# Kernel tuning notes

Hardware: AMD Instinct MI355X
Metric: run time of the kernel (lower is better)

Reference implementation:

```python
import jax, jax.numpy as jnp
import numpy as np

B, N, C, D = 16, 1024, 768, 384

def setup_inputs() -> dict:
    key = jax.random.key(0)
    ks = jax.random.split(key, 12)
    s_in = 1.0 / np.sqrt(C)
    s_d = 1.0 / np.sqrt(D)
    return {
        "x": jax.random.normal(ks[0], (B, N, C), dtype=jnp.float32),
        "adj": jax.random.uniform(ks[1], (B, N, N), dtype=jnp.float32),
        "W_theta": jax.random.uniform(ks[2], (C, D), minval=-s_in, maxval=s_in),
        "b_theta": jax.random.uniform(ks[3], (D,), minval=-s_in, maxval=s_in),
        "W_phi": jax.random.uniform(ks[4], (C, D), minval=-s_in, maxval=s_in),
        "b_phi": jax.random.uniform(ks[5], (D,), minval=-s_in, maxval=s_in),
        "W_g": jax.random.uniform(ks[6], (C, D), minval=-s_in, maxval=s_in),
        "b_g": jax.random.uniform(ks[7], (D,), minval=-s_in, maxval=s_in),
        "W_out": jax.random.uniform(ks[8], (D, C), minval=-s_d, maxval=s_d),
        "b_out": jax.random.uniform(ks[9], (C,), minval=-s_d, maxval=s_d),
    }

def reference(x, adj, W_theta, b_theta, W_phi, b_phi, W_g, b_g, W_out, b_out):
    # projections: [B,N,C] @ [C,D] -> [B,N,D]
    theta = x @ W_theta + b_theta
    phi = x @ W_phi + b_phi
    g = x @ W_g + b_g
    # unscaled attention scores with multiplicative adjacency mask
    attn = jnp.einsum('bnd,bmd->bnm', theta, phi) * adj  # [B,N,N]
    attn = jax.nn.softmax(attn, axis=-1)  # dropout is identity in eval mode
    out = jnp.einsum('bnm,bmd->bnd', attn, g)  # [B,N,D]
    out = out @ W_out + b_out  # [B,N,C]
    return out + x
```

## Files before the change

### kernel.cpp

```cpp
#include <hip/hip_runtime.h>
#include <hip/hip_bf16.h>

typedef __hip_bfloat16 bf16;
typedef short bf16x8 __attribute__((ext_vector_type(8)));
typedef float f32x4 __attribute__((ext_vector_type(4)));

constexpr int Bb = 16, Nn = 1024, Cc = 768, Dd = 384;

static __device__ __forceinline__ f32x4 mfma16(bf16x8 a, bf16x8 b, f32x4 c) {
    return __builtin_amdgcn_mfma_f32_16x16x32_bf16(a, b, c, 0, 0, 0);
}
static __device__ __forceinline__ short f2b(float v) {
    __hip_bfloat16 h = __float2bfloat16(v);
    return *reinterpret_cast<short*>(&h);
}
static __device__ __forceinline__ unsigned pack2(float lo, float hi) {
    return ((unsigned)(unsigned short)f2b(hi) << 16) | (unsigned short)(unsigned)f2b(lo);
}
static __device__ __forceinline__ float b2f(bf16 x) { return __bfloat162float(x); }

__global__ __launch_bounds__(256) void cast_bias(
    const float* __restrict__ in, uint4* __restrict__ out,
    const float* __restrict__ bt, const float* __restrict__ bp,
    const float* __restrict__ bg, float* __restrict__ biasP)
{
    const size_t i = (size_t)blockIdx.x * 256 + threadIdx.x;
    const float4 a = reinterpret_cast<const float4*>(in)[i * 2];
    const float4 b = reinterpret_cast<const float4*>(in)[i * 2 + 1];
    uint4 v;
    v.x = pack2(a.x, a.y);
    v.y = pack2(a.z, a.w);
    v.z = pack2(b.x, b.y);
    v.w = pack2(b.z, b.w);
    out[i] = v;
    if (blockIdx.x == 0) {
        for (int k = threadIdx.x; k < 1152; k += 256)
            biasP[k] = k < 384 ? bt[k] : (k < 768 ? bp[k - 384] : bg[k - 768]);
    }
}

__global__ __launch_bounds__(256) void transpose_cast(
    const float* __restrict__ in, bf16* __restrict__ out, int K, int N)
{
    __shared__ float t[32][33];
    const int n0 = blockIdx.x * 32, k0 = blockIdx.y * 32;
    const int tx = threadIdx.x & 31, ty = threadIdx.x >> 5;
#pragma unroll
    for (int i = 0; i < 4; i++)
        t[ty + i * 8][tx] = in[(size_t)(k0 + ty + i * 8) * N + n0 + tx];
    __syncthreads();
#pragma unroll
    for (int i = 0; i < 4; i++)
        out[(size_t)(n0 + ty + i * 8) * K + k0 + tx] = __float2bfloat16(t[tx][ty + i * 8]);
}

__global__ __launch_bounds__(256) void transpose_cast3(
    const float* __restrict__ w0, const float* __restrict__ w1,
    const float* __restrict__ w2, bf16* __restrict__ outbase)
{
    __shared__ float t[32][33];
    const float* in = blockIdx.z == 0 ? w0 : (blockIdx.z == 1 ? w1 : w2);
    bf16* out = outbase + (size_t)blockIdx.z * Cc * Dd;
    const int n0 = blockIdx.x * 32, k0 = blockIdx.y * 32;
    const int tx = threadIdx.x & 31, ty = threadIdx.x >> 5;
#pragma unroll
    for (int i = 0; i < 4; i++)
        t[ty + i * 8][tx] = in[(size_t)(k0 + ty + i * 8) * Dd + n0 + tx];
    __syncthreads();
#pragma unroll
    for (int i = 0; i < 4; i++)
        out[(size_t)(n0 + ty + i * 8) * Cc + k0 + tx] = __float2bfloat16(t[tx][ty + i * 8]);
}

template <typename TA, int EPI>
__global__ __launch_bounds__(256) void gemm_mfma(
    const TA* __restrict__ A, const bf16* __restrict__ BT,
    const float* __restrict__ bias, const float* __restrict__ resid,
    void* __restrict__ outp, int K, int Nout)
{
    __shared__ short As[128 * 40];
    __shared__ short Bs[128 * 40];
    const int tid = threadIdx.x;
    const int lane = tid & 63, w = tid >> 6;
    const int quad = lane >> 4, c = lane & 15;
    const int row0 = blockIdx.x * 128, col0 = blockIdx.y * 128;
    const int wm = (w & 1) * 64, wn = (w >> 1) * 64;

    const f32x4 fz = {0.f, 0.f, 0.f, 0.f};
    f32x4 acc[4][4];
#pragma unroll
    for (int i = 0; i < 4; i++)
#pragma unroll
        for (int j = 0; j < 4; j++) acc[i][j] = fz;

    for (int k0 = 0; k0 < K; k0 += 32) {
        __syncthreads();
        if (sizeof(TA) == 4) {
            const float* Af = (const float*)A;
#pragma unroll
            for (int u = 0; u < 4; u++) {
                const int id = u * 256 + tid;
                const int r = id >> 3, c4 = (id & 7) * 4;
                const float4 v = *reinterpret_cast<const float4*>(Af + (size_t)(row0 + r) * K + k0 + c4);
                uint2 p;
                p.x = pack2(v.x, v.y);
                p.y = pack2(v.z, v.w);
                *reinterpret_cast<uint2*>(&As[r * 40 + c4]) = p;
            }
        } else {
            const bf16* Ab = (const bf16*)A;
#pragma unroll
            for (int u = 0; u < 2; u++) {
                const int id = u * 256 + tid;
                const int r = id >> 2, c8 = (id & 3) * 8;
                const uint4 v = *reinterpret_cast<const uint4*>(Ab + (size_t)(row0 + r) * K + k0 + c8);
                *reinterpret_cast<uint4*>(&As[r * 40 + c8]) = v;
            }
        }
#pragma unroll
        for (int u = 0; u < 2; u++) {
            const int id = u * 256 + tid;
            const int r = id >> 2, c8 = (id & 3) * 8;
            const uint4 v = *reinterpret_cast<const uint4*>(BT + (size_t)(col0 + r) * K + k0 + c8);
            *reinterpret_cast<uint4*>(&Bs[r * 40 + c8]) = v;
        }
        __syncthreads();

        bf16x8 af[4], bfr[4];
#pragma unroll
        for (int i = 0; i < 4; i++)
            af[i] = *reinterpret_cast<const bf16x8*>(&As[(wm + i * 16 + c) * 40 + quad * 8]);
#pragma unroll
        for (int j = 0; j < 4; j++)
            bfr[j] = *reinterpret_cast<const bf16x8*>(&Bs[(wn + j * 16 + c) * 40 + quad * 8]);
#pragma unroll
        for (int i = 0; i < 4; i++)
#pragma unroll
            for (int j = 0; j < 4; j++)
                acc[i][j] = mfma16(af[i], bfr[j], acc[i][j]);
    }

    const size_t SZc = (size_t)Bb * Nn * Dd;
#pragma unroll
    for (int i = 0; i < 4; i++) {
        const int rowb = row0 + wm + i * 16 + quad * 4;
#pragma unroll
        for (int j = 0; j < 4; j++) {
            const int col = col0 + wn + j * 16 + c;
            const float bcol = bias[col];
#pragma unroll
            for (int r = 0; r < 4; r++) {
                float v = acc[i][j][r] + bcol;
                const int rr = rowb + r;
                if (EPI == 0) {
                    ((bf16*)outp)[(size_t)rr * Nout + col] = __float2bfloat16(v);
                } else if (EPI == 1) {
                    const int bb = rr >> 10, m = rr & 1023;
                    ((bf16*)outp)[((size_t)(bb * Nout + col)) * 1024 + m] = __float2bfloat16(v);
                } else if (EPI == 2) {
                    v += resid[(size_t)rr * Nout + col];
                    ((float*)outp)[(size_t)rr * Nout + col] = v;
                } else {
                    const int seg = col / 384;
                    const int cl = col - seg * 384;
                    bf16* base = (bf16*)outp;
                    if (seg < 2) {
                        base[(size_t)seg * SZc + (size_t)rr * Dd + cl] = __float2bfloat16(v);
                    } else {
                        const int bb = rr >> 10, m = rr & 1023;
                        base[2 * SZc + ((size_t)(bb * Dd + cl)) * 1024 + m] = __float2bfloat16(v);
                    }
                }
            }
        }
    }
}

template <int SPLIT>
__global__ __launch_bounds__(256, 2) void flash_attn(
    const bf16* __restrict__ theta, const bf16* __restrict__ phi,
    const bf16* __restrict__ gT, const float* __restrict__ adj,
    bf16* __restrict__ O, float* __restrict__ Sp, float* __restrict__ ml)
{
    __shared__ short phs[32 * 392];
    __shared__ short gts[192 * 64];

    const int tid = threadIdx.x;
    const int lane = tid & 63, w = tid >> 6;
    const int quad = lane >> 4, c = lane & 15;
    const int qb = blockIdx.x, b = blockIdx.y;
    const int sp = (SPLIT > 1) ? blockIdx.z : 0;
    constexpr int CH = Nn / SPLIT;
    const int n_lo = sp * CH;

    const size_t thbase = ((size_t)b * Nn + qb * 64 + w * 16 + c) * Dd;
    bf16x8 ath[12];
#pragma unroll
    for (int dq = 0; dq < 12; dq++)
        ath[dq] = *reinterpret_cast<const bf16x8*>(theta + thbase + dq * 32 + quad * 8);

    const int goff = (c >> 1) * 64 + (((4 * (c & 1) + quad) ^ ((c >> 1) & 7)) * 8);

    const f32x4 fz = {0.f, 0.f, 0.f, 0.f};
    f32x4 o[24];
#pragma unroll
    for (int t = 0; t < 24; t++) o[t] = fz;
    float mrow[4], lrow[4];
#pragma unroll
    for (int r = 0; r < 4; r++) { mrow[r] = -INFINITY; lrow[r] = 0.f; }

    for (int it = 0; it < CH / 32; ++it) {
        const int n0 = n_lo + it * 32;
        __syncthreads();
        {
            const bf16* src = phi + ((size_t)b * Nn + n0) * Dd;
#pragma unroll
            for (int u = 0; u < 6; u++) {
                const int id = u * 256 + tid;
                const int r = id / 48, cc = (id % 48) * 8;
                const uint4 v = *reinterpret_cast<const uint4*>(src + (size_t)r * Dd + cc);
                *reinterpret_cast<uint4*>(&phs[r * 392 + cc]) = v;
            }
        }
        {
            const bf16* src = gT + ((size_t)b * Dd) * Nn + n0;
#pragma unroll
            for (int u = 0; u < 6; u++) {
                const int id = u * 256 + tid;
                const int r = id >> 3, sl = id & 7;
                const int sg = sl ^ (r & 7);
                const int d = 2 * r + (sg >> 2), cc = (sg & 3) * 8;
                const uint4 v = *reinterpret_cast<const uint4*>(src + (size_t)d * Nn + cc);
                *reinterpret_cast<uint4*>(&gts[id * 8]) = v;
            }
        }
        __syncthreads();

        f32x4 s0 = fz, s1 = fz;
#pragma unroll
        for (int dq = 0; dq < 12; dq++) {
            const bf16x8 b0 = *reinterpret_cast<const bf16x8*>(&phs[c * 392 + dq * 32 + quad * 8]);
            const bf16x8 b1 = *reinterpret_cast<const bf16x8*>(&phs[(16 + c) * 392 + dq * 32 + quad * 8]);
            s0 = mfma16(ath[dq], b0, s0);
            s1 = mfma16(ath[dq], b1, s1);
        }

        const float* arow = adj + ((size_t)b * Nn + qb * 64 + w * 16 + quad * 4) * Nn + n0;
        float p0[4], p1[4], alpha[4];
#pragma unroll
        for (int r = 0; r < 4; r++) {
            const float v0 = s0[r] * arow[(size_t)r * Nn + c];
            const float v1 = s1[r] * arow[(size_t)r * Nn + 16 + c];
            float t = fmaxf(v0, v1);
#pragma unroll
            for (int msk = 1; msk < 16; msk <<= 1) t = fmaxf(t, __shfl_xor(t, msk));
            const float mn = fmaxf(mrow[r], t);
            alpha[r] = __expf(mrow[r] - mn);
            mrow[r] = mn;
            p0[r] = __expf(v0 - mn);
            p1[r] = __expf(v1 - mn);
            float u = p0[r] + p1[r];
#pragma unroll
            for (int msk = 1; msk < 16; msk <<= 1) u += __shfl_xor(u, msk);
            lrow[r] = lrow[r] * alpha[r] + u;
        }
#pragma unroll
        for (int t = 0; t < 24; t++)
#pragma unroll
            for (int r = 0; r < 4; r++) o[t][r] *= alpha[r];

        __syncthreads();
        short* pl = phs + w * 640;
#pragma unroll
        for (int r = 0; r < 4; r++) {
            pl[(quad * 4 + r) * 40 + c] = f2b(p0[r]);
            pl[(quad * 4 + r) * 40 + 16 + c] = f2b(p1[r]);
        }
        const bf16x8 ap = *reinterpret_cast<const bf16x8*>(&pl[c * 40 + quad * 8]);
#pragma unroll
        for (int dn = 0; dn < 24; dn++) {
            const bf16x8 bg = *reinterpret_cast<const bf16x8*>(&gts[dn * 512 + goff]);
            o[dn] = mfma16(ap, bg, o[dn]);
        }
    }

    const int rowb = qb * 64 + w * 16 + quad * 4;
    if (SPLIT > 1) {
        float* srow = Sp + ((size_t)sp * Bb * Nn + (size_t)b * Nn + rowb) * Dd;
#pragma unroll
        for (int dn = 0; dn < 24; dn++)
#pragma unroll
            for (int r = 0; r < 4; r++)
                srow[(size_t)r * Dd + dn * 16 + c] = o[dn][r];
        if (c == 0) {
#pragma unroll
            for (int r = 0; r < 4; r++) {
                const size_t rid = (size_t)sp * Bb * Nn + (size_t)b * Nn + rowb + r;
                ml[rid * 2]     = mrow[r];
                ml[rid * 2 + 1] = lrow[r];
            }
        }
    } else {
        float inv[4];
#pragma unroll
        for (int r = 0; r < 4; r++) inv[r] = 1.0f / lrow[r];
        bf16* orow = O + ((size_t)b * Nn + rowb) * Dd;
#pragma unroll
        for (int dn = 0; dn < 24; dn++)
#pragma unroll
            for (int r = 0; r < 4; r++)
                orow[(size_t)r * Dd + dn * 16 + c] = __float2bfloat16(o[dn][r] * inv[r]);
    }
}

template <int NS>
__global__ __launch_bounds__(256) void attn_combine(
    const float* __restrict__ Sp, const float* __restrict__ ml,
    bf16* __restrict__ O)
{
    constexpr size_t M = (size_t)Bb * Nn;
    const size_t idx = (size_t)blockIdx.x * 256 + threadIdx.x;
    const size_t e0 = idx * 4;
    const size_t row = e0 / Dd;
    float mv[NS], lv[NS];
    float mx = -INFINITY;
#pragma unroll
    for (int i = 0; i < NS; i++) {
        mv[i] = ml[((size_t)i * M + row) * 2];
        lv[i] = ml[((size_t)i * M + row) * 2 + 1];
        mx = fmaxf(mx, mv[i]);
    }
    float wsum = 0.f, wv[NS];
#pragma unroll
    for (int i = 0; i < NS; i++) { wv[i] = __expf(mv[i] - mx); wsum += wv[i] * lv[i]; }
    const float inv = 1.0f / wsum;
    float ax = 0.f, ay = 0.f, az = 0.f, aw = 0.f;
#pragma unroll
    for (int i = 0; i < NS; i++) {
        const float4 a = *reinterpret_cast<const float4*>(Sp + (size_t)i * M * Dd + e0);
        ax += wv[i] * a.x; ay += wv[i] * a.y; az += wv[i] * a.z; aw += wv[i] * a.w;
    }
    uint2 p;
    p.x = pack2(ax * inv, ay * inv);
    p.y = pack2(az * inv, aw * inv);
    *reinterpret_cast<uint2*>(O + e0) = p;
}

__global__ __launch_bounds__(256) void proj_gemm(
    const float* __restrict__ A, const float* __restrict__ W,
    const float* __restrict__ bias, bf16* __restrict__ out,
    int M, int K, int Nd)
{
    __shared__ float Asm[16][65];
    __shared__ float Bsm[16][65];
    const int tid = threadIdx.x;
    const int tx = tid & 15, ty = tid >> 4;
    const int row0 = blockIdx.x * 64, col0 = blockIdx.y * 64;
    float acc[4][4] = {};
    for (int k0 = 0; k0 < K; k0 += 16) {
        {
            const int m = tid >> 2, kq = (tid & 3) * 4;
            const float* p = A + (size_t)(row0 + m) * K + k0 + kq;
#pragma unroll
            for (int j = 0; j < 4; j++) Asm[kq + j][m] = p[j];
        }
        {
            const int k = tid >> 4, n4 = (tid & 15) * 4;
            const float* p = W + (size_t)(k0 + k) * Nd + col0 + n4;
#pragma unroll
            for (int j = 0; j < 4; j++) Bsm[k][n4 + j] = p[j];
        }
        __syncthreads();
#pragma unroll
        for (int k = 0; k < 16; k++) {
            float a[4], bv[4];
#pragma unroll
            for (int j = 0; j < 4; j++) a[j] = Asm[k][ty * 4 + j];
#pragma unroll
            for (int j = 0; j < 4; j++) bv[j] = Bsm[k][tx * 4 + j];
#pragma unroll
            for (int i = 0; i < 4; i++)
#pragma unroll
                for (int j = 0; j < 4; j++) acc[i][j] += a[i] * bv[j];
        }
        __syncthreads();
    }
#pragma unroll
    for (int i = 0; i < 4; i++) {
        const int row = row0 + ty * 4 + i;
#pragma unroll
        for (int j = 0; j < 4; j++) {
            const int col = col0 + tx * 4 + j;
            out[(size_t)row * Nd + col] = __float2bfloat16(acc[i][j] + bias[col]);
        }
    }
}

__global__ __launch_bounds__(256) void fused_attn(
    const float* __restrict__ x, const float* __restrict__ adj,
    const float* __restrict__ W_theta, const float* __restrict__ b_theta,
    const bf16* __restrict__ phi, const bf16* __restrict__ g,
    const float* __restrict__ W_out, const float* __restrict__ b_out,
    float* __restrict__ out)
{
    __shared__ float xs[Cc];
    __shared__ float th[Dd];
    __shared__ float s[Nn];
    __shared__ float Os[Dd];
    __shared__ float red[256];
    const int tid = threadIdx.x;
    const int n = blockIdx.x, b = blockIdx.y;
    const int lane = tid & 63, wave = tid >> 6;
    const size_t row = (size_t)b * Nn + n;
    const size_t baseD = (size_t)b * Nn * Dd;
    for (int c = tid; c < Cc; c += 256) xs[c] = x[row * Cc + c];
    __syncthreads();
    for (int d = tid; d < Dd; d += 256) {
        float acc = b_theta[d];
#pragma unroll 8
        for (int c = 0; c < Cc; c++) acc += xs[c] * W_theta[(size_t)c * Dd + d];
        th[d] = acc;
    }
    __syncthreads();
    for (int m = wave; m < Nn; m += 4) {
        const bf16* prow = phi + baseD + (size_t)m * Dd;
        float partial = 0.f;
#pragma unroll
        for (int j = 0; j < 6; j++) {
            const int d = lane + 64 * j;
            partial += th[d] * b2f(prow[d]);
        }
#pragma unroll
        for (int off = 32; off > 0; off >>= 1) partial += __shfl_down(partial, off);
        if (lane == 0)
            s[m] = partial * adj[(size_t)b * Nn * Nn + (size_t)n * Nn + m];
    }
    __syncthreads();
    float mx = -1e30f;
    for (int i = tid; i < Nn; i += 256) mx = fmaxf(mx, s[i]);
    red[tid] = mx; __syncthreads();
    for (int st = 128; st > 0; st >>= 1) {
        if (tid < st) red[tid] = fmaxf(red[tid], red[tid + st]);
        __syncthreads();
    }
    mx = red[0]; __syncthreads();
    float lsum = 0.f;
    for (int i = tid; i < Nn; i += 256) {
        const float e = __expf(s[i] - mx);
        s[i] = e;
        lsum += e;
    }
    red[tid] = lsum; __syncthreads();
    for (int st = 128; st > 0; st >>= 1) {
        if (tid < st) red[tid] += red[tid + st];
        __syncthreads();
    }
    const float inv = 1.0f / red[0];
    __syncthreads();
    for (int d = tid; d < Dd; d += 256) {
        float acc = 0.f;
#pragma unroll 8
        for (int m = 0; m < Nn; m++) acc += s[m] * b2f(g[baseD + (size_t)m * Dd + d]);
        Os[d] = acc * inv;
    }
    __syncthreads();
    for (int c = tid; c < Cc; c += 256) {
        float acc = b_out[c] + xs[c];
#pragma unroll 8
        for (int d = 0; d < Dd; d++) acc += Os[d] * W_out[(size_t)d * Cc + c];
        out[row * Cc + c] = acc;
    }
}

extern "C" void kernel_launch(void* const* d_in, const int* in_sizes, int n_in,
                              void* d_out, int out_size, void* d_ws, size_t ws_size,
                              hipStream_t stream)
{
    const float* x       = (const float*)d_in[0];
    const float* adj     = (const float*)d_in[1];
    const float* W_theta = (const float*)d_in[2];
    const float* b_theta = (const float*)d_in[3];
    const float* W_phi   = (const float*)d_in[4];
    const float* b_phi   = (const float*)d_in[5];
    const float* W_g     = (const float*)d_in[6];
    const float* b_g     = (const float*)d_in[7];
    const float* W_out   = (const float*)d_in[8];
    const float* b_out   = (const float*)d_in[9];
    float* out = (float*)d_out;

    const int M = Bb * Nn;
    const size_t SZ  = (size_t)Bb * Nn * Dd;
    const size_t SZX = (size_t)M * Cc;
    const size_t WSZ = (size_t)Cc * Dd;
    const size_t NEED_OLD = (4 * WSZ + 4 * SZ) * sizeof(bf16);
    const size_t NEED_NEW = (4 * WSZ + 4 * SZ + SZX) * sizeof(bf16)
                          + 1152 * sizeof(float);
    const size_t NEED_S2 = NEED_NEW + (2 * SZ + 4 * (size_t)M) * sizeof(float);
    const size_t NEED_S4 = NEED_NEW + (4 * SZ + 8 * (size_t)M) * sizeof(float);

    dim3 blk(256);

    if (ws_size >= NEED_NEW) {
        bf16* WtT   = (bf16*)d_ws;
        bf16* WoT   = WtT + 3 * WSZ;
        bf16* theta = WoT + WSZ;
        bf16* phi   = theta + SZ;
        bf16* gT    = phi + SZ;
        bf16* O     = gT + SZ;
        bf16* xb    = O + SZ;
        float* biasP = (float*)(xb + SZX);
        float* Sp    = biasP + 1152;
        float* mlp   = Sp + 4 * SZ;

        cast_bias<<<dim3((unsigned)(SZX / 2048)), blk, 0, stream>>>(
            x, (uint4*)xb, b_theta, b_phi, b_g, biasP);
        transpose_cast3<<<dim3(Dd / 32, Cc / 32, 3), blk, 0, stream>>>(
            W_theta, W_phi, W_g, WtT);
        transpose_cast<<<dim3(Cc / 32, Dd / 32), blk, 0, stream>>>(W_out, WoT, Dd, Cc);

        gemm_mfma<bf16, 3><<<dim3(M / 128, 1152 / 128), blk, 0, stream>>>(
            xb, WtT, biasP, nullptr, theta, Cc, 1152);

        if (ws_size >= NEED_S4) {
            flash_attn<4><<<dim3(Nn / 64, Bb, 4), blk, 0, stream>>>(
                theta, phi, gT, adj, nullptr, Sp, mlp);
            attn_combine<4><<<dim3((unsigned)(SZ / 1024)), blk, 0, stream>>>(Sp, mlp, O);
        } else if (ws_size >= NEED_S2) {
            float* mlp2 = Sp + 2 * SZ;
            flash_attn<2><<<dim3(Nn / 64, Bb, 2), blk, 0, stream>>>(
                theta, phi, gT, adj, nullptr, Sp, mlp2);
            attn_combine<2><<<dim3((unsigned)(SZ / 1024)), blk, 0, stream>>>(Sp, mlp2, O);
        } else {
            flash_attn<1><<<dim3(Nn / 64, Bb, 1), blk, 0, stream>>>(
                theta, phi, gT, adj, O, nullptr, nullptr);
        }

        gemm_mfma<bf16, 2><<<dim3(M / 128, Cc / 128), blk, 0, stream>>>(
            O, WoT, b_out, x, out, Dd, Cc);
    } else if (ws_size >= NEED_OLD) {
        bf16* WtT   = (bf16*)d_ws;
        bf16* WpT   = WtT + WSZ;
        bf16* WgT   = WtT + 2 * WSZ;
        bf16* WoT   = WtT + 3 * WSZ;
        bf16* theta = WoT + WSZ;
        bf16* phi   = theta + SZ;
        bf16* gT    = phi + SZ;
        bf16* O     = gT + SZ;

        transpose_cast<<<dim3(Dd / 32, Cc / 32), blk, 0, stream>>>(W_theta, WtT, Cc, Dd);
        transpose_cast<<<dim3(Dd / 32, Cc / 32), blk, 0, stream>>>(W_phi,   WpT, Cc, Dd);
        transpose_cast<<<dim3(Dd / 32, Cc / 32), blk, 0, stream>>>(W_g,     WgT, Cc, Dd);
        transpose_cast<<<dim3(Cc / 32, Dd / 32), blk, 0, stream>>>(W_out,   WoT, Dd, Cc);

        dim3 gp(M / 128, Dd / 128);
        gemm_mfma<float, 0><<<gp, blk, 0, stream>>>(x, WtT, b_theta, nullptr, theta, Cc, Dd);
        gemm_mfma<float, 0><<<gp, blk, 0, stream>>>(x, WpT, b_phi,   nullptr, phi,   Cc, Dd);
        gemm_mfma<float, 1><<<gp, blk, 0, stream>>>(x, WgT, b_g,     nullptr, gT,    Cc, Dd);

        flash_attn<1><<<dim3(Nn / 64, Bb, 1), blk, 0, stream>>>(
            theta, phi, gT, adj, O, nullptr, nullptr);

        dim3 go(M / 128, Cc / 128);
        gemm_mfma<bf16, 2><<<go, blk, 0, stream>>>(O, WoT, b_out, x, out, Dd, Cc);
    } else {
        bf16* phi = (bf16*)d_ws;
        bf16* g   = phi + SZ;
        dim3 gproj(M / 64, Dd / 64);
        proj_gemm<<<gproj, blk, 0, stream>>>(x, W_phi, b_phi, phi, M, Cc, Dd);
        proj_gemm<<<gproj, blk, 0, stream>>>(x, W_g, b_g, g, M, Cc, Dd);
        fused_attn<<<dim3(Nn, Bb), blk, 0, stream>>>(
            x, adj, W_theta, b_theta, phi, g, W_out, b_out, out);
    }
}
```

Before: 354.0 us.

## Add direct global-to-LDS bf16 GEMM with XOR swizzle and drop split-4 attention

Adds a new bf16 GEMM kernel that loads A and B tiles straight into LDS with global_load_lds, using a K-step of 64 and an XOR-swizzled layout to avoid bank conflicts. This replaces the register-staged path used for the QKV projection and output GEMMs. It also removes the split-4 attention path, so the default runs split-2 attention with its combine step, which changes how much parallelism the attention stage has. The new GEMM keeps the two-barrier, single-buffer scheme, so loads still do not overlap with compute.

```diff
diff --git a/kernel.cpp b/kernel.cpp
--- a/kernel.cpp
+++ b/kernel.cpp
@@ -18,6 +18,10 @@
     return ((unsigned)(unsigned short)f2b(hi) << 16) | (unsigned short)(unsigned)f2b(lo);
 }
 static __device__ __forceinline__ float b2f(bf16 x) { return __bfloat162float(x); }
+
+#define GLOAD_LDS16(g, l) __builtin_amdgcn_global_load_lds(                    \
+    (const __attribute__((address_space(1))) void*)(g),                        \
+    (__attribute__((address_space(3))) void*)(l), 16, 0, 0)
 
 __global__ __launch_bounds__(256) void cast_bias(
     const float* __restrict__ in, uint4* __restrict__ out,
@@ -72,20 +76,27 @@
         out[(size_t)(n0 + ty + i * 8) * Cc + k0 + tx] = __float2bfloat16(t[tx][ty + i * 8]);
 }
 
-template <typename TA, int EPI>
-__global__ __launch_bounds__(256) void gemm_mfma(
-    const TA* __restrict__ A, const bf16* __restrict__ BT,
+template <int EPI>
+__global__ __launch_bounds__(256) void gemm_bf16(
+    const bf16* __restrict__ A, const bf16* __restrict__ BT,
     const float* __restrict__ bias, const float* __restrict__ resid,
     void* __restrict__ outp, int K, int Nout)
 {
-    __shared__ short As[128 * 40];
-    __shared__ short Bs[128 * 40];
+    __shared__ short As[128 * 64];
+    __shared__ short Bs[128 * 64];
     const int tid = threadIdx.x;
     const int lane = tid & 63, w = tid >> 6;
     const int quad = lane >> 4, c = lane & 15;
     const int row0 = blockIdx.x * 128, col0 = blockIdx.y * 128;
     const int wm = (w & 1) * 64, wn = (w >> 1) * 64;
 
+    const int rA = w * 32 + (lane >> 3);
+    const int cs = (lane & 7) ^ (lane >> 3);
+    const bf16* Ag = A  + (size_t)(row0 + rA) * K + cs * 8;
+    const bf16* Bg = BT + (size_t)(col0 + rA) * K + cs * 8;
+    char* Asb = (char*)As + w * 4096;
+    char* Bsb = (char*)Bs + w * 4096;
+
     const f32x4 fz = {0.f, 0.f, 0.f, 0.f};
     f32x4 acc[4][4];
 #pragma unroll
@@ -93,51 +104,38 @@
 #pragma unroll
         for (int j = 0; j < 4; j++) acc[i][j] = fz;
 
-    for (int k0 = 0; k0 < K; k0 += 32) {
-        __syncthreads();
-        if (sizeof(TA) == 4) {
-            const float* Af = (const float*)A;
-#pragma unroll
-            for (int u = 0; u < 4; u++) {
-                const int id = u * 256 + tid;
-                const int r = id >> 3, c4 = (id & 7) * 4;
-                const float4 v = *reinterpret_cast<const float4*>(Af + (size_t)(row0 + r) * K + k0 + c4);
-                uint2 p;
-                p.x = pack2(v.x, v.y);
-                p.y = pack2(v.z, v.w);
-                *reinterpret_cast<uint2*>(&As[r * 40 + c4]) = p;
-            }
-        } else {
-            const bf16* Ab = (const bf16*)A;
-#pragma unroll
-            for (int u = 0; u < 2; u++) {
-                const int id = u * 256 + tid;
-                const int r = id >> 2, c8 = (id & 3) * 8;
-                const uint4 v = *reinterpret_cast<const uint4*>(Ab + (size_t)(row0 + r) * K + k0 + c8);
-                *reinterpret_cast<uint4*>(&As[r * 40 + c8]) = v;
-            }
-        }
-#pragma unroll
-        for (int u = 0; u < 2; u++) {
-            const int id = u * 256 + tid;
-            const int r = id >> 2, c8 = (id & 3) * 8;
-            const uint4 v = *reinterpret_cast<const uint4*>(BT + (size_t)(col0 + r) * K + k0 + c8);
-            *reinterpret_cast<uint4*>(&Bs[r * 40 + c8]) = v;
-        }
-        __syncthreads();
-
-        bf16x8 af[4], bfr[4];
-#pragma unroll
-        for (int i = 0; i < 4; i++)
-            af[i] = *reinterpret_cast<const bf16x8*>(&As[(wm + i * 16 + c) * 40 + quad * 8]);
-#pragma unroll
-        for (int j = 0; j < 4; j++)
-            bfr[j] = *reinterpret_cast<const bf16x8*>(&Bs[(wn + j * 16 + c) * 40 + quad * 8]);
-#pragma unroll
-        for (int i = 0; i < 4; i++)
-#pragma unroll
-            for (int j = 0; j < 4; j++)
-                acc[i][j] = mfma16(af[i], bfr[j], acc[i][j]);
+    for (int k0 = 0; k0 < K; k0 += 64) {
+        __syncthreads();
+#pragma unroll
+        for (int i = 0; i < 4; i++) {
+            GLOAD_LDS16(Ag + (size_t)i * 8 * K + k0, Asb + i * 1024);
+            GLOAD_LDS16(Bg + (size_t)i * 8 * K + k0, Bsb + i * 1024);
+        }
+        __syncthreads();
+
+        bf16x8 af[2][4], bfr[2][4];
+#pragma unroll
+        for (int kk = 0; kk < 2; kk++) {
+#pragma unroll
+            for (int i = 0; i < 4; i++) {
+                const int r = wm + i * 16 + c;
+                const int ch = (kk * 4 + quad) ^ (r & 7);
+                af[kk][i] = *reinterpret_cast<const bf16x8*>(&As[r * 64 + ch * 8]);
+            }
+#pragma unroll
+            for (int j = 0; j < 4; j++) {
+                const int r = wn + j * 16 + c;
+                const int ch = (kk * 4 + quad) ^ (r & 7);
+                bfr[kk][j] = *reinterpret_cast<const bf16x8*>(&Bs[r * 64 + ch * 8]);
+            }
+        }
+#pragma unroll
+        for (int kk = 0; kk < 2; kk++)
+#pragma unroll
+            for (int i = 0; i < 4; i++)
+#pragma unroll
+                for (int j = 0; j < 4; j++)
+                    acc[i][j] = mfma16(af[kk][i], bfr[kk][j], acc[i][j]);
     }
 
     const size_t SZc = (size_t)Bb * Nn * Dd;
@@ -152,12 +150,7 @@
             for (int r = 0; r < 4; r++) {
                 float v = acc[i][j][r] + bcol;
                 const int rr = rowb + r;
-                if (EPI == 0) {
-                    ((bf16*)outp)[(size_t)rr * Nout + col] = __float2bfloat16(v);
-                } else if (EPI == 1) {
-                    const int bb = rr >> 10, m = rr & 1023;
-                    ((bf16*)outp)[((size_t)(bb * Nout + col)) * 1024 + m] = __float2bfloat16(v);
-                } else if (EPI == 2) {
+                if (EPI == 2) {
                     v += resid[(size_t)rr * Nout + col];
                     ((float*)outp)[(size_t)rr * Nout + col] = v;
                 } else {
@@ -170,6 +163,99 @@
                         const int bb = rr >> 10, m = rr & 1023;
                         base[2 * SZc + ((size_t)(bb * Dd + cl)) * 1024 + m] = __float2bfloat16(v);
                     }
+                }
+            }
+        }
+    }
+}
+
+template <typename TA, int EPI>
+__global__ __launch_bounds__(256) void gemm_mfma(
+    const TA* __restrict__ A, const bf16* __restrict__ BT,
+    const float* __restrict__ bias, const float* __restrict__ resid,
+    void* __restrict__ outp, int K, int Nout)
+{
+    __shared__ short As[128 * 40];
+    __shared__ short Bs[128 * 40];
+    const int tid = threadIdx.x;
+    const int lane = tid & 63, w = tid >> 6;
+    const int quad = lane >> 4, c = lane & 15;
+    const int row0 = blockIdx.x * 128, col0 = blockIdx.y * 128;
+    const int wm = (w & 1) * 64, wn = (w >> 1) * 64;
+
+    const f32x4 fz = {0.f, 0.f, 0.f, 0.f};
+    f32x4 acc[4][4];
+#pragma unroll
+    for (int i = 0; i < 4; i++)
+#pragma unroll
+        for (int j = 0; j < 4; j++) acc[i][j] = fz;
+
+    for (int k0 = 0; k0 < K; k0 += 32) {
+        __syncthreads();
+        if (sizeof(TA) == 4) {
+            const float* Af = (const float*)A;
+#pragma unroll
+            for (int u = 0; u < 4; u++) {
+                const int id = u * 256 + tid;
+                const int r = id >> 3, c4 = (id & 7) * 4;
+                const float4 v = *reinterpret_cast<const float4*>(Af + (size_t)(row0 + r) * K + k0 + c4);
+                uint2 p;
+                p.x = pack2(v.x, v.y);
+                p.y = pack2(v.z, v.w);
+                *reinterpret_cast<uint2*>(&As[r * 40 + c4]) = p;
+            }
+        } else {
+            const bf16* Ab = (const bf16*)A;
+#pragma unroll
+            for (int u = 0; u < 2; u++) {
+                const int id = u * 256 + tid;
+                const int r = id >> 2, c8 = (id & 3) * 8;
+                const uint4 v = *reinterpret_cast<const uint4*>(Ab + (size_t)(row0 + r) * K + k0 + c8);
+                *reinterpret_cast<uint4*>(&As[r * 40 + c8]) = v;
+            }
+        }
+#pragma unroll
+        for (int u = 0; u < 2; u++) {
+            const int id = u * 256 + tid;
+            const int r = id >> 2, c8 = (id & 3) * 8;
+            const uint4 v = *reinterpret_cast<const uint4*>(BT + (size_t)(col0 + r) * K + k0 + c8);
+            *reinterpret_cast<uint4*>(&Bs[r * 40 + c8]) = v;
+        }
+        __syncthreads();
+
+        bf16x8 af[4], bfr[4];
+#pragma unroll
+        for (int i = 0; i < 4; i++)
+            af[i] = *reinterpret_cast<const bf16x8*>(&As[(wm + i * 16 + c) * 40 + quad * 8]);
+#pragma unroll
+        for (int j = 0; j < 4; j++)
+            bfr[j] = *reinterpret_cast<const bf16x8*>(&Bs[(wn + j * 16 + c) * 40 + quad * 8]);
+#pragma unroll
+        for (int i = 0; i < 4; i++)
+#pragma unroll
+            for (int j = 0; j < 4; j++)
+                acc[i][j] = mfma16(af[i], bfr[j], acc[i][j]);
+    }
+
+#pragma unroll
+    for (int i = 0; i < 4; i++) {
+        const int rowb = row0 + wm + i * 16 + quad * 4;
+#pragma unroll
+        for (int j = 0; j < 4; j++) {
+            const int col = col0 + wn + j * 16 + c;
+            const float bcol = bias[col];
+#pragma unroll
+            for (int r = 0; r < 4; r++) {
+                float v = acc[i][j][r] + bcol;
+                const int rr = rowb + r;
+                if (EPI == 0) {
+                    ((bf16*)outp)[(size_t)rr * Nout + col] = __float2bfloat16(v);
+                } else if (EPI == 1) {
+                    const int bb = rr >> 10, m = rr & 1023;
+                    ((bf16*)outp)[((size_t)(bb * Nout + col)) * 1024 + m] = __float2bfloat16(v);
+                } else {
+                    v += resid[(size_t)rr * Nout + col];
+                    ((float*)outp)[(size_t)rr * Nout + col] = v;
                 }
             }
         }
@@ -496,7 +582,6 @@
     const size_t NEED_NEW = (4 * WSZ + 4 * SZ + SZX) * sizeof(bf16)
                           + 1152 * sizeof(float);
     const size_t NEED_S2 = NEED_NEW + (2 * SZ + 4 * (size_t)M) * sizeof(float);
-    const size_t NEED_S4 = NEED_NEW + (4 * SZ + 8 * (size_t)M) * sizeof(float);
 
     dim3 blk(256);
 
@@ -510,7 +595,7 @@
         bf16* xb    = O + SZ;
         float* biasP = (float*)(xb + SZX);
         float* Sp    = biasP + 1152;
-        float* mlp   = Sp + 4 * SZ;
+        float* mlp   = Sp + 2 * SZ;
 
         cast_bias<<<dim3((unsigned)(SZX / 2048)), blk, 0, stream>>>(
             x, (uint4*)xb, b_theta, b_phi, b_g, biasP);
@@ -518,24 +603,19 @@
             W_theta, W_phi, W_g, WtT);
         transpose_cast<<<dim3(Cc / 32, Dd / 32), blk, 0, stream>>>(W_out, WoT, Dd, Cc);
 
-        gemm_mfma<bf16, 3><<<dim3(M / 128, 1152 / 128), blk, 0, stream>>>(
+        gemm_bf16<3><<<dim3(M / 128, 1152 / 128), blk, 0, stream>>>(
             xb, WtT, biasP, nullptr, theta, Cc, 1152);
 
-        if (ws_size >= NEED_S4) {
-            flash_attn<4><<<dim3(Nn / 64, Bb, 4), blk, 0, stream>>>(
+        if (ws_size >= NEED_S2) {
+            flash_attn<2><<<dim3(Nn / 64, Bb, 2), blk, 0, stream>>>(
                 theta, phi, gT, adj, nullptr, Sp, mlp);
-            attn_combine<4><<<dim3((unsigned)(SZ / 1024)), blk, 0, stream>>>(Sp, mlp, O);
-        } else if (ws_size >= NEED_S2) {
-            float* mlp2 = Sp + 2 * SZ;
-            flash_attn<2><<<dim3(Nn / 64, Bb, 2), blk, 0, stream>>>(
-                theta, phi, gT, adj, nullptr, Sp, mlp2);
-            attn_combine<2><<<dim3((unsigned)(SZ / 1024)), blk, 0, stream>>>(Sp, mlp2, O);
+            attn_combine<2><<<dim3((unsigned)(SZ / 1024)), blk, 0, stream>>>(Sp, mlp, O);
         } else {
             flash_attn<1><<<dim3(Nn / 64, Bb, 1), blk, 0, stream>>>(
                 theta, phi, gT, adj, O, nullptr, nullptr);
         }
 
-        gemm_mfma<bf16, 2><<<dim3(M / 128, Cc / 128), blk, 0, stream>>>(
+        gemm_bf16<2><<<dim3(M / 128, Cc / 128), blk, 0, stream>>>(
             O, WoT, b_out, x, out, Dd, Cc);
     } else if (ws_size >= NEED_OLD) {
         bf16* WtT   = (bf16*)d_ws;
```

Measured after the change: 320.6 us. 1.1x faster.
